# Performance work log

Hardware: AMD Instinct MI355X
Metric: run time of the kernel (lower is better)

## Reference

```python
import jax, jax.numpy as jnp
import numpy as np

D_MODEL = 512
N_HEADS = 8
EDGE_FEAT_DIM = 4
NUM_GRAPHS = 64
NODES_PER_GRAPH = 128
N_NODES = NUM_GRAPHS * NODES_PER_GRAPH          # 8192
EDGES_PER_GRAPH = 4096                           # avg degree 32
N_EDGES = NUM_GRAPHS * EDGES_PER_GRAPH           # 262144


def setup_inputs() -> dict:
    key = jax.random.key(0)
    ks = jax.random.split(key, 12)
    s = 0.02
    x = jax.random.normal(ks[0], (N_NODES, D_MODEL), jnp.float32)
    # edges constrained within their graph (block-diagonal structure)
    g_of_e = jnp.arange(N_EDGES, dtype=jnp.int32) // EDGES_PER_GRAPH
    src = g_of_e * NODES_PER_GRAPH + jax.random.randint(ks[1], (N_EDGES,), 0, NODES_PER_GRAPH, jnp.int32)
    dst = g_of_e * NODES_PER_GRAPH + jax.random.randint(ks[2], (N_EDGES,), 0, NODES_PER_GRAPH, jnp.int32)
    edge_index = jnp.stack([src, dst]).astype(jnp.int32)
    edge_attr = jax.random.normal(ks[3], (N_EDGES, EDGE_FEAT_DIM), jnp.float32)
    batch = jnp.repeat(jnp.arange(NUM_GRAPHS, dtype=jnp.int32), NODES_PER_GRAPH)
    # projection weights (in,out) convention: y = x @ W + b
    Wq = jax.random.normal(ks[4], (D_MODEL, D_MODEL), jnp.float32) * s
    Wk = jax.random.normal(ks[5], (D_MODEL, D_MODEL), jnp.float32) * s
    Wv = jax.random.normal(ks[6], (D_MODEL, D_MODEL), jnp.float32) * s
    Wo = jax.random.normal(ks[7], (D_MODEL, D_MODEL), jnp.float32) * s
    bq = jnp.zeros((D_MODEL,), jnp.float32)
    bk = jnp.zeros((D_MODEL,), jnp.float32)
    bv = jnp.zeros((D_MODEL,), jnp.float32)
    bo = jnp.zeros((D_MODEL,), jnp.float32)
    # edge bias MLP: edge_feat_dim -> d_model -> n_heads
    W1 = jax.random.normal(ks[8], (EDGE_FEAT_DIM, D_MODEL), jnp.float32) * s
    b1 = jnp.zeros((D_MODEL,), jnp.float32)
    W2 = jax.random.normal(ks[9], (D_MODEL, N_HEADS), jnp.float32) * s
    b2 = jnp.zeros((N_HEADS,), jnp.float32)
    return {"x": x, "edge_index": edge_index, "edge_attr": edge_attr, "batch": batch,
            "n_g": NODES_PER_GRAPH,
            "Wq": Wq, "bq": bq, "Wk": Wk, "bk": bk, "Wv": Wv, "bv": bv,
            "Wo": Wo, "bo": bo, "W1": W1, "b1": b1, "W2": W2, "b2": b2}


def reference(x, edge_index, edge_attr, batch, n_g, Wq, bq, Wk, bk, Wv, bv, Wo, bo, W1, b1, W2, b2):
    # batch is contiguous equal-size blocks of n_g nodes per graph, so the
    # per-graph Python loop of the original collapses to a batched (G, n_g)
    # block-diagonal attention. Dropout is identity (eval / p used only in train).
    N, d_model = x.shape
    H = W2.shape[1]
    d_k = d_model // H
    G = N // n_g
    scale = 1.0 / float(np.sqrt(d_k))

    Q = (x @ Wq + bq).reshape(G, n_g, H, d_k)
    K = (x @ Wk + bk).reshape(G, n_g, H, d_k)
    V = (x @ Wv + bv).reshape(G, n_g, H, d_k)

    # (G, i, j, h) dense per-graph scores
    scores = jnp.einsum('gihd,gjhd->gijh', Q, K) * scale

    # edge bias: MLP(edge_attr) -> (E, H), scattered at (graph, local_src, local_dst)
    bias = jax.nn.relu(edge_attr @ W1 + b1) @ W2 + b2
    ge = edge_index[0] // n_g
    ls = edge_index[0] % n_g
    ld = edge_index[1] % n_g
    scores = scores.at[ge, ls, ld].add(bias)

    attn = jax.nn.softmax(scores, axis=2)  # softmax over j (keys), matches dim=1 of (i,j,h)
    out = jnp.einsum('gijh,gjhd->gihd', attn, V).reshape(N, d_model)
    return out @ Wo + bo
```

## Files before the change

kernel.cpp:

```cpp
#include <hip/hip_runtime.h>
#include <hip/hip_bf16.h>

#define E_TOTAL 262144
#define NG      128
#define GRAPHS  64
#define NHEADS  8
#define DKH     64
#define DMODEL  512
#define NNODES  8192

typedef __bf16 bf16x8 __attribute__((ext_vector_type(8)));
typedef __bf16 bf16x4 __attribute__((ext_vector_type(4)));
typedef float  f32x4  __attribute__((ext_vector_type(4)));
typedef short  s16x4  __attribute__((ext_vector_type(4)));

typedef __attribute__((address_space(3))) char lds_char;
typedef const __attribute__((address_space(1))) char glb_char;

__device__ inline __hip_bfloat16 f2hbf(float f) { return __float2bfloat16(f); }
__device__ inline unsigned short f2u16(float f) {
    return __builtin_bit_cast(unsigned short, __float2bfloat16(f));
}
__device__ inline __bf16 f2bf(float f) {
    return __builtin_bit_cast(__bf16, f2u16(f));
}
__device__ inline bf16x8 cvt8(float4 lo, float4 hi) {
    bf16x8 o;
    o[0] = f2bf(lo.x); o[1] = f2bf(lo.y); o[2] = f2bf(lo.z); o[3] = f2bf(lo.w);
    o[4] = f2bf(hi.x); o[5] = f2bf(hi.y); o[6] = f2bf(hi.z); o[7] = f2bf(hi.w);
    return o;
}

__global__ __launch_bounds__(256) void prep_kernel(
    const float* __restrict__ Wq, const float* __restrict__ Wk,
    const float* __restrict__ Wv, const float* __restrict__ Wo,
    const float* __restrict__ W1, const float* __restrict__ b1,
    const float* __restrict__ W2, const float* __restrict__ b2,
    const float* __restrict__ x, __hip_bfloat16* __restrict__ xbf,
    __hip_bfloat16* __restrict__ wqkvt, __hip_bfloat16* __restrict__ wot,
    __hip_bfloat16* __restrict__ w1fragt, float* __restrict__ b1f,
    __hip_bfloat16* __restrict__ w2at, float* __restrict__ b2f)
{
    int blk = blockIdx.x, tid = threadIdx.x;
    if (blk < 256) {
        __shared__ __align__(16) __hip_bfloat16 tile[64][65];
        const float* src;
        __hip_bfloat16* dstT;
        int n0, k0, nb;
        if (blk < 192) {
            int nt = blk % 24, ktile = blk / 24;
            n0 = nt * 64; k0 = ktile * 64;
            if (n0 < 512)       { src = Wq; nb = n0; }
            else if (n0 < 1024) { src = Wk; nb = n0 - 512; }
            else                { src = Wv; nb = n0 - 1024; }
            dstT = wqkvt;
        } else {
            int t = blk - 192;
            n0 = (t % 8) * 64; k0 = (t / 8) * 64; nb = n0;
            src = Wo; dstT = wot;
        }
        #pragma unroll
        for (int i = 0; i < 16; ++i) {
            int idx = tid + i * 256;
            int kr = idx >> 6, nc = idx & 63;
            tile[kr][nc] = f2hbf(src[(size_t)(k0 + kr) * 512 + nb + nc]);
        }
        __syncthreads();
        #pragma unroll
        for (int i = 0; i < 16; ++i) {
            int idx = tid + i * 256;
            int nr = idx >> 6, kc = idx & 63;
            dstT[(size_t)(n0 + nr) * 512 + k0 + kc] = tile[kc][nr];
        }
    } else if (blk == 256) {
        __hip_bfloat16 z = f2hbf(0.f);
        for (int n = tid; n < 512; n += 256) {
            #pragma unroll
            for (int j = 0; j < 4; ++j) w1fragt[n * 4 + j] = f2hbf(W1[(size_t)j * 512 + n]);
        }
        for (int i = tid; i < 512; i += 256) b1f[i] = b1[i];
        for (int i = tid; i < 32 * 64 * 4; i += 256) {
            int t = i >> 8, lane = (i >> 2) & 63, j = i & 3;
            int q = lane >> 4, l = lane & 15;
            w2at[i] = (l < 8) ? f2hbf(W2[(size_t)(16 * t + 4 * q + j) * 8 + l]) : z;
        }
        if (tid < 8) b2f[tid] = b2[tid];
    } else {
        int base = (blk - 257) * 2048 + tid * 8;
        float4 lo = *(const float4*)(x + base);
        float4 hi = *(const float4*)(x + base + 4);
        *(bf16x8*)(xbf + base) = cvt8(lo, hi);
    }
}

template <bool QKPATH>
__device__ __forceinline__ void gemm0_body(
    const __hip_bfloat16* __restrict__ A, const __hip_bfloat16* __restrict__ BT,
    int row0, int col0,
    const float* __restrict__ bq, const float* __restrict__ bk,
    const float* __restrict__ bv,
    __hip_bfloat16* __restrict__ qbuf, __hip_bfloat16* __restrict__ kbuf,
    __hip_bfloat16* __restrict__ vt,
    __hip_bfloat16* __restrict__ As, __hip_bfloat16* __restrict__ Bs)
{
    const int K = 512;
    int tid = threadIdx.x;
    int lane = tid & 63, quad = lane >> 4, l16 = lane & 15;
    int wave = tid >> 6;
    int wi = wave >> 1, wj = wave & 1;

    f32x4 acc[2][4];
    #pragma unroll
    for (int a = 0; a < 2; a++)
        #pragma unroll
        for (int b = 0; b < 4; b++)
            #pragma unroll
            for (int r = 0; r < 4; r++) acc[a][b][r] = 0.f;

    const __hip_bfloat16* Ag = A + (size_t)(row0 + (tid >> 2)) * K + (tid & 3) * 8;
    const __hip_bfloat16* Bg = BT + (size_t)(col0 + (tid >> 2)) * K + (tid & 3) * 8;
    char* AsB = (char*)As;
    char* BsB = (char*)Bs;

#define G0STAGE(kt, buf) do { \
    __builtin_amdgcn_global_load_lds((glb_char*)(Ag + (kt) * 32), (lds_char*)(AsB + (buf) * 8192 + tid * 16), 16, 0, 0); \
    __builtin_amdgcn_global_load_lds((glb_char*)(Bg + (kt) * 32), (lds_char*)(BsB + (buf) * 8192 + tid * 16), 16, 0, 0); \
} while (0)

    G0STAGE(0, 0);
    G0STAGE(1, 1);

    #pragma unroll
    for (int kt = 0; kt < 16; ++kt) {
        if (kt < 15) asm volatile("s_waitcnt vmcnt(2)" ::: "memory");
        else         asm volatile("s_waitcnt vmcnt(0)" ::: "memory");
        __builtin_amdgcn_s_barrier();
        if (kt < 14) G0STAGE(kt + 2, (kt + 2) % 3);
        const __hip_bfloat16* Asc = As + (kt % 3) * 4096;
        const __hip_bfloat16* Bsc = Bs + (kt % 3) * 4096;
        bf16x8 af[2], bfr[4];
        #pragma unroll
        for (int t = 0; t < 2; t++)
            af[t] = *(const bf16x8*)&Asc[(wi * 32 + t * 16 + l16) * 32 + quad * 8];
        #pragma unroll
        for (int t = 0; t < 4; t++)
            bfr[t] = *(const bf16x8*)&Bsc[(wj * 64 + t * 16 + l16) * 32 + quad * 8];
        #pragma unroll
        for (int ti = 0; ti < 2; ti++)
            #pragma unroll
            for (int tj = 0; tj < 4; tj++) {
                if constexpr (QKPATH)
                    acc[ti][tj] = __builtin_amdgcn_mfma_f32_16x16x32_bf16(bfr[tj], af[ti], acc[ti][tj], 0, 0, 0);
                else
                    acc[ti][tj] = __builtin_amdgcn_mfma_f32_16x16x32_bf16(af[ti], bfr[tj], acc[ti][tj], 0, 0, 0);
            }
    }
#undef G0STAGE

    if constexpr (QKPATH) {
        int g = row0 >> 7;
        int ibase = wi * 32 + l16;
        int cb0 = col0 + wj * 64 + quad * 4;
        bool isQ = (col0 < 512);
        const float* bias = isQ ? bq : bk;
        int boff = isQ ? 0 : 512;
        __hip_bfloat16* dstbuf = isQ ? qbuf : kbuf;
        #pragma unroll
        for (int tj = 0; tj < 4; tj++) {
            int cb = cb0 + tj * 16;
            float4 bb = *(const float4*)(bias + cb - boff);
            int c = cb - boff;
            int hh = c >> 6, d = c & 63;
            __hip_bfloat16* dst = dstbuf + ((size_t)(g * 8 + hh) * 128) * 64 + d;
            #pragma unroll
            for (int ti = 0; ti < 2; ti++) {
                int i = ibase + ti * 16;
                bf16x4 v;
                v[0] = f2bf(acc[ti][tj][0] + bb.x);
                v[1] = f2bf(acc[ti][tj][1] + bb.y);
                v[2] = f2bf(acc[ti][tj][2] + bb.z);
                v[3] = f2bf(acc[ti][tj][3] + bb.w);
                *(bf16x4*)(dst + (size_t)i * 64) = v;
            }
        }
    } else {
        int g = row0 >> 7;
        int i0 = wi * 32 + quad * 4;
        #pragma unroll
        for (int tj = 0; tj < 4; tj++) {
            int c = col0 - 1024 + wj * 64 + tj * 16 + l16;
            int hh = c >> 6, d = c & 63;
            float bvv = bv[c];
            __hip_bfloat16* vdst = vt + ((size_t)(g * 8 + hh) * 64 + d) * 128 + i0;
            #pragma unroll
            for (int ti = 0; ti < 2; ti++) {
                bf16x4 v;
                v[0] = f2bf(acc[ti][tj][0] + bvv);
                v[1] = f2bf(acc[ti][tj][1] + bvv);
                v[2] = f2bf(acc[ti][tj][2] + bvv);
                v[3] = f2bf(acc[ti][tj][3] + bvv);
                *(bf16x4*)(vdst + ti * 16) = v;
            }
        }
    }
}

__device__ __forceinline__ void edge_body(
    int eblk,
    const float* __restrict__ ea,
    const __hip_bfloat16* w1s, const float* b1s, const __hip_bfloat16* w2s,
    const float* __restrict__ b2f,
    float* __restrict__ biasE)
{
    int tid = threadIdx.x, wave = tid >> 6, lane = tid & 63;
    int quad = lane >> 4, l16 = lane & 15;
    int eb = eblk * 512 + wave * 64;

    s16x4 eaf[4] = {};
    if (quad == 0) {
        #pragma unroll
        for (int gg = 0; gg < 4; ++gg) {
            float4 e4 = *(const float4*)(ea + (size_t)(eb + gg * 16 + l16) * 4);
            eaf[gg][0] = (short)f2u16(e4.x); eaf[gg][1] = (short)f2u16(e4.y);
            eaf[gg][2] = (short)f2u16(e4.z); eaf[gg][3] = (short)f2u16(e4.w);
        }
    }

    f32x4 c2[4];
    #pragma unroll
    for (int gg = 0; gg < 4; ++gg)
        #pragma unroll
        for (int r = 0; r < 4; ++r) c2[gg][r] = 0.f;

    #pragma unroll 4
    for (int t = 0; t < 32; ++t) {
        s16x4 a1 = *(const s16x4*)(w1s + ((size_t)t * 16 + l16) * 4);
        float4 b14 = *(const float4*)(b1s + t * 16 + quad * 4);
        s16x4 a2 = *(const s16x4*)(w2s + ((size_t)t * 64 + lane) * 4);
        #pragma unroll
        for (int gg = 0; gg < 4; ++gg) {
            f32x4 c1;
            c1[0] = b14.x; c1[1] = b14.y; c1[2] = b14.z; c1[3] = b14.w;
            c1 = __builtin_amdgcn_mfma_f32_16x16x16bf16_1k(a1, eaf[gg], c1, 0, 0, 0);
            s16x4 hfrag;
            hfrag[0] = (short)f2u16(fmaxf(c1[0], 0.f));
            hfrag[1] = (short)f2u16(fmaxf(c1[1], 0.f));
            hfrag[2] = (short)f2u16(fmaxf(c1[2], 0.f));
            hfrag[3] = (short)f2u16(fmaxf(c1[3], 0.f));
            c2[gg] = __builtin_amdgcn_mfma_f32_16x16x16bf16_1k(a2, hfrag, c2[gg], 0, 0, 0);
        }
    }
    if (quad < 2) {
        #pragma unroll
        for (int gg = 0; gg < 4; ++gg) {
            #pragma unroll
            for (int r = 0; r < 4; ++r) {
                int hh = quad * 4 + r;
                biasE[(size_t)hh * E_TOTAL + eb + gg * 16 + l16] = c2[gg][r] + b2f[hh];
            }
        }
    }
}

__global__ __launch_bounds__(512) void mega_kernel(
    const __hip_bfloat16* __restrict__ A, const __hip_bfloat16* __restrict__ BT,
    const float* __restrict__ bq, const float* __restrict__ bk,
    const float* __restrict__ bv,
    __hip_bfloat16* __restrict__ qbuf, __hip_bfloat16* __restrict__ kbuf,
    __hip_bfloat16* __restrict__ vt,
    const float* __restrict__ ea,
    const char* __restrict__ tabg,
    const float* __restrict__ b2f,
    float* __restrict__ biasE)
{
    __shared__ __align__(16) __hip_bfloat16 As[3 * 128 * 32];
    __shared__ __align__(16) __hip_bfloat16 Bs[3 * 128 * 32];
    int blk0 = blockIdx.x;
    int blk = (blk0 & 7) * 160 + (blk0 >> 3);
    int u = blk / 5, v = blk % 5;
    if (v < 3) {
        int tile = u * 3 + v;
        int row0 = (tile & 63) * 128, col0 = (tile >> 6) * 128;
        if (col0 < 1024)
            gemm0_body<true>(A, BT, row0, col0, bq, bk, bv, qbuf, kbuf, vt, As, Bs);
        else
            gemm0_body<false>(A, BT, row0, col0, bq, bk, bv, qbuf, kbuf, vt, As, Bs);
    } else {
        int tid = threadIdx.x;
        int4* dst = (int4*)As;
        const int4* srcv = (const int4*)tabg;
        #pragma unroll
        for (int i = 0; i < 3; ++i) {
            int idx = tid + i * 512;
            if (idx < 1408) dst[idx] = srcv[idx];
        }
        __syncthreads();
        const __hip_bfloat16* w1s = (const __hip_bfloat16*)As;
        const float* b1s = (const float*)((const char*)As + 0x1000);
        const __hip_bfloat16* w2s = (const __hip_bfloat16*)((const char*)As + 0x1800);
        edge_body(u * 2 + (v - 3), ea, w1s, b1s, w2s, b2f, biasE);
    }
}

__global__ __launch_bounds__(256) void gemm1_kernel(
    const __hip_bfloat16* __restrict__ A, const __hip_bfloat16* __restrict__ BT,
    const float* __restrict__ bo, float* __restrict__ out)
{
    const int K = 512;
    __shared__ __align__(16) __hip_bfloat16 As[3 * 128 * 32];
    __shared__ __align__(16) __hip_bfloat16 Bs[3 * 64 * 32];
    int tid = threadIdx.x;
    int lane = tid & 63, quad = lane >> 4, l16 = lane & 15;
    int wave = tid >> 6, wi = wave >> 1, wj = wave & 1;
    int row0 = blockIdx.x * 128, col0 = blockIdx.y * 64;

    f32x4 acc[4][2];
    #pragma unroll
    for (int a = 0; a < 4; a++)
        #pragma unroll
        for (int b = 0; b < 2; b++)
            #pragma unroll
            for (int r = 0; r < 4; r++) acc[a][b][r] = 0.f;

    const __hip_bfloat16* Ag0 = A + (size_t)(row0 + (tid >> 2)) * K + (tid & 3) * 8;
    const __hip_bfloat16* Ag1 = Ag0 + (size_t)64 * K;
    const __hip_bfloat16* Bg  = BT + (size_t)(col0 + (tid >> 2)) * K + (tid & 3) * 8;
    char* AsB = (char*)As;
    char* BsB = (char*)Bs;

#define G1STAGE(kt, buf) do { \
    __builtin_amdgcn_global_load_lds((glb_char*)(Ag0 + (kt) * 32), (lds_char*)(AsB + (buf) * 8192 + tid * 16), 16, 0, 0); \
    __builtin_amdgcn_global_load_lds((glb_char*)(Ag1 + (kt) * 32), (lds_char*)(AsB + (buf) * 8192 + 4096 + tid * 16), 16, 0, 0); \
    __builtin_amdgcn_global_load_lds((glb_char*)(Bg + (kt) * 32),  (lds_char*)(BsB + (buf) * 4096 + tid * 16), 16, 0, 0); \
} while (0)

    G1STAGE(0, 0);
    G1STAGE(1, 1);

    #pragma unroll
    for (int kt = 0; kt < 16; ++kt) {
        if (kt < 15) asm volatile("s_waitcnt vmcnt(3)" ::: "memory");
        else         asm volatile("s_waitcnt vmcnt(0)" ::: "memory");
        __builtin_amdgcn_s_barrier();
        if (kt < 14) G1STAGE(kt + 2, (kt + 2) % 3);
        const __hip_bfloat16* Asc = As + (kt % 3) * 4096;
        const __hip_bfloat16* Bsc = Bs + (kt % 3) * 2048;
        bf16x8 af[4], bfr[2];
        #pragma unroll
        for (int t = 0; t < 4; t++)
            af[t] = *(const bf16x8*)&Asc[(wi * 64 + t * 16 + l16) * 32 + quad * 8];
        #pragma unroll
        for (int t = 0; t < 2; t++)
            bfr[t] = *(const bf16x8*)&Bsc[(wj * 32 + t * 16 + l16) * 32 + quad * 8];
        #pragma unroll
        for (int ti = 0; ti < 4; ti++)
            #pragma unroll
            for (int tj = 0; tj < 2; tj++)
                acc[ti][tj] = __builtin_amdgcn_mfma_f32_16x16x32_bf16(bfr[tj], af[ti], acc[ti][tj], 0, 0, 0);
    }
#undef G1STAGE

    int rbase = row0 + wi * 64 + l16;
    int cb0 = col0 + wj * 32 + quad * 4;
    #pragma unroll
    for (int tj = 0; tj < 2; tj++) {
        int cb = cb0 + tj * 16;
        float4 bb = *(const float4*)(bo + cb);
        #pragma unroll
        for (int ti = 0; ti < 4; ti++) {
            int row = rbase + ti * 16;
            f32x4 v;
            v[0] = acc[ti][tj][0] + bb.x;
            v[1] = acc[ti][tj][1] + bb.y;
            v[2] = acc[ti][tj][2] + bb.z;
            v[3] = acc[ti][tj][3] + bb.w;
            *(f32x4*)(out + (size_t)row * 512 + cb) = v;
        }
    }
}

#define SS 132
__global__ __launch_bounds__(512) void attn_kernel(
    const __hip_bfloat16* __restrict__ qbuf,
    const __hip_bfloat16* __restrict__ kbuf,
    const __hip_bfloat16* __restrict__ vt,
    const float* __restrict__ biasE,
    const int* __restrict__ eidx,
    __hip_bfloat16* __restrict__ O)
{
    __shared__ __align__(16) float S[128 * SS];
    int blk = blockIdx.x, g = blk & 63, h = blk >> 6;
    int tid = threadIdx.x, wave = tid >> 6, lane = tid & 63;
    int quad = lane >> 4, l16 = lane & 15;

    int   sa[8];
    float bvv[8];
    #pragma unroll
    for (int u = 0; u < 8; ++u) {
        int idx = g * 4096 + tid + u * 512;
        int ls = eidx[idx] & 127;
        int ld = eidx[E_TOTAL + idx] & 127;
        sa[u] = ls * SS + ld;
        bvv[u] = biasE[(size_t)h * E_TOTAL + idx];
    }

    const __hip_bfloat16* qbase = qbuf + (size_t)(g * 8 + h) * 128 * 64;
    const __hip_bfloat16* kbase = kbuf + (size_t)(g * 8 + h) * 128 * 64;
    const __hip_bfloat16* vbase = vt + (size_t)(g * 8 + h) * 64 * 128;

    f32x4 acc[8];
    #pragma unroll
    for (int j = 0; j < 8; j++)
        #pragma unroll
        for (int r = 0; r < 4; r++) acc[j][r] = 0.f;

    #pragma unroll
    for (int k0 = 0; k0 < 64; k0 += 32) {
        int m = wave * 16 + l16;
        bf16x8 af = *(const bf16x8*)(qbase + (size_t)m * 64 + k0 + quad * 8);
        #pragma unroll
        for (int tj = 0; tj < 8; tj++) {
            int n = tj * 16 + l16;
            bf16x8 bfr = *(const bf16x8*)(kbase + (size_t)n * 64 + k0 + quad * 8);
            acc[tj] = __builtin_amdgcn_mfma_f32_16x16x32_bf16(bfr, af, acc[tj], 0, 0, 0);
        }
    }
    {
        int i = wave * 16 + l16;
        #pragma unroll
        for (int tj = 0; tj < 8; tj++) {
            f32x4 sv;
            sv[0] = acc[tj][0] * 0.125f;
            sv[1] = acc[tj][1] * 0.125f;
            sv[2] = acc[tj][2] * 0.125f;
            sv[3] = acc[tj][3] * 0.125f;
            *(f32x4*)&S[i * SS + tj * 16 + quad * 4] = sv;
        }
    }

    bf16x8 vpre[8];
    #pragma unroll
    for (int kh = 0; kh < 2; kh++)
        #pragma unroll
        for (int tj = 0; tj < 4; tj++)
            vpre[kh * 4 + tj] = *(const bf16x8*)(vbase + (size_t)(tj * 16 + l16) * 128 + kh * 32 + quad * 8);

    __syncthreads();

    #pragma unroll
    for (int u = 0; u < 8; ++u)
        atomicAdd(&S[sa[u]], bvv[u]);
    __syncthreads();

    #pragma unroll 4
    for (int r = wave * 16; r < wave * 16 + 16; ++r) {
        float2 v = *(const float2*)&S[r * SS + 2 * lane];
        float m = fmaxf(v.x, v.y);
        #pragma unroll
        for (int off = 32; off > 0; off >>= 1) m = fmaxf(m, __shfl_xor(m, off));
        float e0 = __expf(v.x - m), e1 = __expf(v.y - m);
        float s = e0 + e1;
        #pragma unroll
        for (int off = 32; off > 0; off >>= 1) s += __shfl_xor(s, off);
        float inv = 1.0f / s;
        float2 o; o.x = e0 * inv; o.y = e1 * inv;
        *(float2*)&S[r * SS + 2 * lane] = o;
    }
    __syncthreads();

    f32x4 oacc[4];
    #pragma unroll
    for (int j = 0; j < 4; j++)
        #pragma unroll
        for (int r = 0; r < 4; r++) oacc[j][r] = 0.f;

    #pragma unroll
    for (int k0 = 0; k0 < 128; k0 += 32) {
        int m = wave * 16 + l16;
        const float* p = &S[m * SS + k0 + quad * 8];
        f32x4 xa = *(const f32x4*)p;
        f32x4 xb = *(const f32x4*)(p + 4);
        bf16x8 af;
        af[0] = f2bf(xa[0]); af[1] = f2bf(xa[1]); af[2] = f2bf(xa[2]); af[3] = f2bf(xa[3]);
        af[4] = f2bf(xb[0]); af[5] = f2bf(xb[1]); af[6] = f2bf(xb[2]); af[7] = f2bf(xb[3]);
        #pragma unroll
        for (int tj = 0; tj < 4; tj++) {
            bf16x8 bfr = (k0 < 64)
                ? vpre[(k0 >> 5) * 4 + tj]
                : *(const bf16x8*)(vbase + (size_t)(tj * 16 + l16) * 128 + k0 + quad * 8);
            oacc[tj] = __builtin_amdgcn_mfma_f32_16x16x32_bf16(bfr, af, oacc[tj], 0, 0, 0);
        }
    }
    {
        int i = wave * 16 + l16;
        __hip_bfloat16* obase = O + (size_t)(g * 128 + i) * 512 + h * 64 + quad * 4;
        #pragma unroll
        for (int tj = 0; tj < 4; tj++) {
            bf16x4 ov;
            ov[0] = f2bf(oacc[tj][0]);
            ov[1] = f2bf(oacc[tj][1]);
            ov[2] = f2bf(oacc[tj][2]);
            ov[3] = f2bf(oacc[tj][3]);
            *(bf16x4*)(obase + tj * 16) = ov;
        }
    }
}

#define WS_WQKVT 0x0
#define WS_WOT   0x180000
#define WS_TAB   0x200000
#define WS_W1FR  0x200000
#define WS_B1F   0x201000
#define WS_W2AT  0x201800
#define WS_B2F   0x205800
#define WS_Q     0x210000
#define WS_K     0xA10000
#define WS_VT    0x1210000
#define WS_BIASE 0x1A10000
#define WS_O     0x2210000
#define WS_XBF   WS_O

extern "C" void kernel_launch(void* const* d_in, const int* in_sizes, int n_in,
                              void* d_out, int out_size, void* d_ws, size_t ws_size,
                              hipStream_t stream) {
    const float* x    = (const float*)d_in[0];
    const int*   eidx = (const int*)d_in[1];
    const float* ea   = (const float*)d_in[2];
    const float* Wq = (const float*)d_in[5];
    const float* bq = (const float*)d_in[6];
    const float* Wk = (const float*)d_in[7];
    const float* bk = (const float*)d_in[8];
    const float* Wv = (const float*)d_in[9];
    const float* bv = (const float*)d_in[10];
    const float* Wo = (const float*)d_in[11];
    const float* bo = (const float*)d_in[12];
    const float* W1 = (const float*)d_in[13];
    const float* b1 = (const float*)d_in[14];
    const float* W2 = (const float*)d_in[15];
    const float* b2 = (const float*)d_in[16];

    char* ws = (char*)d_ws;
    __hip_bfloat16* wqkvt   = (__hip_bfloat16*)(ws + WS_WQKVT);
    __hip_bfloat16* wot     = (__hip_bfloat16*)(ws + WS_WOT);
    __hip_bfloat16* w1fragt = (__hip_bfloat16*)(ws + WS_W1FR);
    float* b1f   = (float*)(ws + WS_B1F);
    __hip_bfloat16* w2at    = (__hip_bfloat16*)(ws + WS_W2AT);
    float* b2f   = (float*)(ws + WS_B2F);
    __hip_bfloat16* qbuf = (__hip_bfloat16*)(ws + WS_Q);
    __hip_bfloat16* kbuf = (__hip_bfloat16*)(ws + WS_K);
    __hip_bfloat16* vt  = (__hip_bfloat16*)(ws + WS_VT);
    float* biasE = (float*)(ws + WS_BIASE);
    __hip_bfloat16* O   = (__hip_bfloat16*)(ws + WS_O);
    __hip_bfloat16* xbf = (__hip_bfloat16*)(ws + WS_XBF);

    prep_kernel<<<257 + 2048, 256, 0, stream>>>(Wq, Wk, Wv, Wo, W1, b1, W2, b2,
                                                x, xbf,
                                                wqkvt, wot, w1fragt, b1f, w2at, b2f);
    mega_kernel<<<1280, 512, 0, stream>>>(
        xbf, wqkvt, bq, bk, bv, qbuf, kbuf, vt,
        ea, ws + WS_TAB, b2f, biasE);
    attn_kernel<<<GRAPHS * NHEADS, 512, 0, stream>>>(qbuf, kbuf, vt, biasE, eidx, O);
    gemm1_kernel<<<dim3(NNODES / 128, 512 / 64), 256, 0, stream>>>(
        O, wot, bo, (float*)d_out);
}
```

Baseline: 195.8 us.

## Split mega kernel into separate GEMM and edge kernels; load A fragments directly to registers

Splits the fused GEMM+edge-MLP mega kernel into two launches: a QKV projection kernel and an edge-bias kernel. In the GEMM, the A operand is now loaded straight from global memory into registers, double-buffered one k-step ahead, instead of being staged through LDS. Only B is still staged through LDS with a triple buffer. This halves LDS use per GEMM block, which may allow more resident blocks and removes the A LDS round trip, at the cost of uncoalesced per-lane global loads, an extra kernel launch and the loss of overlap between the GEMM and edge work.

```diff
diff --git a/kernel.cpp b/kernel.cpp
--- a/kernel.cpp
+++ b/kernel.cpp
@@ -101,7 +101,7 @@
     const float* __restrict__ bv,
     __hip_bfloat16* __restrict__ qbuf, __hip_bfloat16* __restrict__ kbuf,
     __hip_bfloat16* __restrict__ vt,
-    __hip_bfloat16* __restrict__ As, __hip_bfloat16* __restrict__ Bs)
+    __hip_bfloat16* __restrict__ Bs)
 {
     const int K = 512;
     int tid = threadIdx.x;
@@ -117,31 +117,31 @@
             #pragma unroll
             for (int r = 0; r < 4; r++) acc[a][b][r] = 0.f;
 
-    const __hip_bfloat16* Ag = A + (size_t)(row0 + (tid >> 2)) * K + (tid & 3) * 8;
+    const __hip_bfloat16* Arow = A + (size_t)(row0 + wi * 32 + l16) * K + quad * 8;
     const __hip_bfloat16* Bg = BT + (size_t)(col0 + (tid >> 2)) * K + (tid & 3) * 8;
-    char* AsB = (char*)As;
     char* BsB = (char*)Bs;
 
-#define G0STAGE(kt, buf) do { \
-    __builtin_amdgcn_global_load_lds((glb_char*)(Ag + (kt) * 32), (lds_char*)(AsB + (buf) * 8192 + tid * 16), 16, 0, 0); \
-    __builtin_amdgcn_global_load_lds((glb_char*)(Bg + (kt) * 32), (lds_char*)(BsB + (buf) * 8192 + tid * 16), 16, 0, 0); \
+#define ALOAD(dst, kt) do { \
+    dst[0] = *(const bf16x8*)(Arow + (kt) * 32); \
+    dst[1] = *(const bf16x8*)(Arow + 16 * K + (kt) * 32); \
 } while (0)
-
-    G0STAGE(0, 0);
-    G0STAGE(1, 1);
+#define BSTAGE(kt, buf) \
+    __builtin_amdgcn_global_load_lds((glb_char*)(Bg + (kt) * 32), (lds_char*)(BsB + (buf) * 8192 + tid * 16), 16, 0, 0)
+
+    bf16x8 afr[2][2];
+    ALOAD(afr[0], 0);
+    BSTAGE(0, 0);
+    BSTAGE(1, 1);
 
     #pragma unroll
     for (int kt = 0; kt < 16; ++kt) {
-        if (kt < 15) asm volatile("s_waitcnt vmcnt(2)" ::: "memory");
+        if (kt < 15) asm volatile("s_waitcnt vmcnt(1)" ::: "memory");
         else         asm volatile("s_waitcnt vmcnt(0)" ::: "memory");
         __builtin_amdgcn_s_barrier();
-        if (kt < 14) G0STAGE(kt + 2, (kt + 2) % 3);
-        const __hip_bfloat16* Asc = As + (kt % 3) * 4096;
+        if (kt < 15) ALOAD(afr[(kt + 1) & 1], kt + 1);
+        if (kt < 14) BSTAGE(kt + 2, (kt + 2) % 3);
         const __hip_bfloat16* Bsc = Bs + (kt % 3) * 4096;
-        bf16x8 af[2], bfr[4];
-        #pragma unroll
-        for (int t = 0; t < 2; t++)
-            af[t] = *(const bf16x8*)&Asc[(wi * 32 + t * 16 + l16) * 32 + quad * 8];
+        bf16x8 bfr[4];
         #pragma unroll
         for (int t = 0; t < 4; t++)
             bfr[t] = *(const bf16x8*)&Bsc[(wj * 64 + t * 16 + l16) * 32 + quad * 8];
@@ -150,12 +150,13 @@
             #pragma unroll
             for (int tj = 0; tj < 4; tj++) {
                 if constexpr (QKPATH)
-                    acc[ti][tj] = __builtin_amdgcn_mfma_f32_16x16x32_bf16(bfr[tj], af[ti], acc[ti][tj], 0, 0, 0);
+                    acc[ti][tj] = __builtin_amdgcn_mfma_f32_16x16x32_bf16(bfr[tj], afr[kt & 1][ti], acc[ti][tj], 0, 0, 0);
                 else
-                    acc[ti][tj] = __builtin_amdgcn_mfma_f32_16x16x32_bf16(af[ti], bfr[tj], acc[ti][tj], 0, 0, 0);
+                    acc[ti][tj] = __builtin_amdgcn_mfma_f32_16x16x32_bf16(afr[kt & 1][ti], bfr[tj], acc[ti][tj], 0, 0, 0);
             }
     }
-#undef G0STAGE
+#undef ALOAD
+#undef BSTAGE
 
     if constexpr (QKPATH) {
         int g = row0 >> 7;
@@ -205,16 +206,45 @@
     }
 }
 
-__device__ __forceinline__ void edge_body(
-    int eblk,
+__global__ __launch_bounds__(512) void gemm0_kernel(
+    const __hip_bfloat16* __restrict__ A, const __hip_bfloat16* __restrict__ BT,
+    const float* __restrict__ bq, const float* __restrict__ bk,
+    const float* __restrict__ bv,
+    __hip_bfloat16* __restrict__ qbuf, __hip_bfloat16* __restrict__ kbuf,
+    __hip_bfloat16* __restrict__ vt)
+{
+    __shared__ __align__(16) __hip_bfloat16 Bs[3 * 128 * 32];
+    int blk = blockIdx.x;
+    int row0 = (blk & 63) * 128, col0 = (blk >> 6) * 128;
+    if (col0 < 1024)
+        gemm0_body<true>(A, BT, row0, col0, bq, bk, bv, qbuf, kbuf, vt, Bs);
+    else
+        gemm0_body<false>(A, BT, row0, col0, bq, bk, bv, qbuf, kbuf, vt, Bs);
+}
+
+__global__ __launch_bounds__(512) void edge_kernel(
     const float* __restrict__ ea,
-    const __hip_bfloat16* w1s, const float* b1s, const __hip_bfloat16* w2s,
+    const char* __restrict__ tabg,
     const float* __restrict__ b2f,
     float* __restrict__ biasE)
 {
+    __shared__ __align__(16) int4 tabs[1408];
     int tid = threadIdx.x, wave = tid >> 6, lane = tid & 63;
     int quad = lane >> 4, l16 = lane & 15;
-    int eb = eblk * 512 + wave * 64;
+    int eb = blockIdx.x * 512 + wave * 64;
+
+    {
+        const int4* srcv = (const int4*)tabg;
+        #pragma unroll
+        for (int i = 0; i < 3; ++i) {
+            int idx = tid + i * 512;
+            if (idx < 1408) tabs[idx] = srcv[idx];
+        }
+    }
+    __syncthreads();
+    const __hip_bfloat16* w1s = (const __hip_bfloat16*)tabs;
+    const float* b1s = (const float*)((const char*)tabs + 0x1000);
+    const __hip_bfloat16* w2s = (const __hip_bfloat16*)((const char*)tabs + 0x1800);
 
     s16x4 eaf[4] = {};
     if (quad == 0) {
@@ -259,46 +289,6 @@
                 biasE[(size_t)hh * E_TOTAL + eb + gg * 16 + l16] = c2[gg][r] + b2f[hh];
             }
         }
-    }
-}
-
-__global__ __launch_bounds__(512) void mega_kernel(
-    const __hip_bfloat16* __restrict__ A, const __hip_bfloat16* __restrict__ BT,
-    const float* __restrict__ bq, const float* __restrict__ bk,
-    const float* __restrict__ bv,
-    __hip_bfloat16* __restrict__ qbuf, __hip_bfloat16* __restrict__ kbuf,
-    __hip_bfloat16* __restrict__ vt,
-    const float* __restrict__ ea,
-    const char* __restrict__ tabg,
-    const float* __restrict__ b2f,
-    float* __restrict__ biasE)
-{
-    __shared__ __align__(16) __hip_bfloat16 As[3 * 128 * 32];
-    __shared__ __align__(16) __hip_bfloat16 Bs[3 * 128 * 32];
-    int blk0 = blockIdx.x;
-    int blk = (blk0 & 7) * 160 + (blk0 >> 3);
-    int u = blk / 5, v = blk % 5;
-    if (v < 3) {
-        int tile = u * 3 + v;
-        int row0 = (tile & 63) * 128, col0 = (tile >> 6) * 128;
-        if (col0 < 1024)
-            gemm0_body<true>(A, BT, row0, col0, bq, bk, bv, qbuf, kbuf, vt, As, Bs);
-        else
-            gemm0_body<false>(A, BT, row0, col0, bq, bk, bv, qbuf, kbuf, vt, As, Bs);
-    } else {
-        int tid = threadIdx.x;
-        int4* dst = (int4*)As;
-        const int4* srcv = (const int4*)tabg;
-        #pragma unroll
-        for (int i = 0; i < 3; ++i) {
-            int idx = tid + i * 512;
-            if (idx < 1408) dst[idx] = srcv[idx];
-        }
-        __syncthreads();
-        const __hip_bfloat16* w1s = (const __hip_bfloat16*)As;
-        const float* b1s = (const float*)((const char*)As + 0x1000);
-        const __hip_bfloat16* w2s = (const __hip_bfloat16*)((const char*)As + 0x1800);
-        edge_body(u * 2 + (v - 3), ea, w1s, b1s, w2s, b2f, biasE);
     }
 }
 
@@ -556,8 +546,9 @@
     prep_kernel<<<257 + 2048, 256, 0, stream>>>(Wq, Wk, Wv, Wo, W1, b1, W2, b2,
                                                 x, xbf,
                                                 wqkvt, wot, w1fragt, b1f, w2at, b2f);
-    mega_kernel<<<1280, 512, 0, stream>>>(
-        xbf, wqkvt, bq, bk, bv, qbuf, kbuf, vt,
+    gemm0_kernel<<<768, 512, 0, stream>>>(
+        xbf, wqkvt, bq, bk, bv, qbuf, kbuf, vt);
+    edge_kernel<<<512, 512, 0, stream>>>(
         ea, ws + WS_TAB, b2f, biasE);
     attn_kernel<<<GRAPHS * NHEADS, 512, 0, stream>>>(qbuf, kbuf, vt, biasE, eidx, O);
     gemm1_kernel<<<dim3(NNODES / 128, 512 / 64), 256, 0, stream>>>(
```

New measurement: 211.6 us. +8.1%, slower.
